# Kernel optimization log

Measured on AMD Instinct MI355X. Metric: run time of the kernel, lower is better.

The kernel has to match this reference:

```python
import jax, jax.numpy as jnp
import numpy as np

T, B, D, R, H = 16, 1024, 1024, 8, 16
DH = D // H


def setup_inputs() -> dict:
    key = jax.random.key(0)
    ks = jax.random.split(key, 10)
    s = 1.0 / np.sqrt(D)
    return {
        "table_embs": jax.random.normal(ks[0], (T, B, D), jnp.float32),
        "rel_embs": jax.random.normal(ks[1], (T, R, D), jnp.float32),
        "rel_idx": jax.random.randint(ks[2], (T, R), 0, T),
        "Wq": jax.random.normal(ks[3], (D, D), jnp.float32) * s,
        "bq": jnp.zeros((D,), jnp.float32),
        "Wk": jax.random.normal(ks[4], (D, D), jnp.float32) * s,
        "bk": jnp.zeros((D,), jnp.float32),
        "Wv": jax.random.normal(ks[5], (D, D), jnp.float32) * s,
        "bv": jnp.zeros((D,), jnp.float32),
        "Wo": jax.random.normal(ks[6], (D, D), jnp.float32) * s,
        "bo": jnp.zeros((D,), jnp.float32),
        "w_rel": jax.random.normal(ks[7], (D,), jnp.float32) * s,
        "b_rel": jnp.zeros((1,), jnp.float32),
    }


def reference(table_embs, rel_embs, rel_idx, Wq, bq, Wk, bk, Wv, bv, Wo, bo, w_rel, b_rel):
    # relationship weights: sigmoid(Linear(rel_emb)) -> scalar per (table, relation)
    rel_w = jax.nn.sigmoid(rel_embs @ w_rel + b_rel[0])          # [T, R]
    # gather related tables' embeddings and apply relationship weight
    others = table_embs[rel_idx]                                  # [T, R, B, D]
    weighted = others * rel_w[:, :, None, None]                   # [T, R, B, D]
    kv_src = jnp.transpose(weighted, (0, 2, 1, 3))                # [T, B, R, D]
    # MultiheadAttention, q_len=1, kv_len=R (PyTorch convention: x @ W.T + b)
    q = (table_embs @ Wq.T + bq).reshape(T, B, H, DH)             # [T, B, H, DH]
    k = (kv_src @ Wk.T + bk).reshape(T, B, R, H, DH)              # [T, B, R, H, DH]
    v = (kv_src @ Wv.T + bv).reshape(T, B, R, H, DH)
    scores = jnp.einsum("tbhd,tbrhd->tbhr", q, k) / np.sqrt(DH)   # [T, B, H, R]
    attn = jax.nn.softmax(scores, axis=-1)
    ctx = jnp.einsum("tbhr,tbrhd->tbhd", attn, v).reshape(T, B, D)
    return ctx @ Wo.T + bo                                        # [T, B, D]
```

## Files before the change

kernel.cpp:

```cpp
#include <hip/hip_runtime.h>


typedef unsigned short u16;
typedef __attribute__((ext_vector_type(8))) short short8;
typedef __attribute__((ext_vector_type(4))) float f32x4;

__device__ __forceinline__ float bf2f(u16 u) {
  unsigned int x = ((unsigned int)u) << 16;
  return __uint_as_float(x);
}
__device__ __forceinline__ u16 f2bf(float f) {
  unsigned int x = __float_as_uint(f);
  unsigned int r = (x + 0x7fffu + ((x >> 16) & 1u)) >> 16;
  return (u16)r;
}

__device__ __forceinline__ void gld_lds16(const void* g, void* l) {
  __builtin_amdgcn_global_load_lds(
      (const __attribute__((address_space(1))) unsigned int*)(unsigned long long)g,
      (__attribute__((address_space(3))) unsigned int*)(unsigned int)(unsigned long long)l,
      16, 0, 0);
}

#define VWAIT(N) asm volatile("s_waitcnt vmcnt(" #N ")" ::: "memory")


__global__ void relw_kernel(const float* __restrict__ rel_embs,
                            const float* __restrict__ w_rel,
                            const float* __restrict__ b_rel,
                            float* __restrict__ rel_w) {
  const int tr = blockIdx.x;
  const float* row = rel_embs + (size_t)tr * 1024;
  const int lane = threadIdx.x;
  float s = 0.f;
  for (int i = lane; i < 1024; i += 64) s += row[i] * w_rel[i];
  for (int off = 32; off > 0; off >>= 1) s += __shfl_down(s, off, 64);
  if (lane == 0) rel_w[tr] = 1.f / (1.f + __expf(-(s + b_rel[0])));
}

__global__ void cvt_f32_bf16(const float* __restrict__ in, u16* __restrict__ out, int n4) {
  int i = blockIdx.x * blockDim.x + threadIdx.x;
  if (i >= n4) return;
  float4 v = ((const float4*)in)[i];
  ushort4 o;
  o.x = f2bf(v.x); o.y = f2bf(v.y); o.z = f2bf(v.z); o.w = f2bf(v.w);
  ((ushort4*)out)[i] = o;
}

__global__ void cvt_w4(const float* __restrict__ Wq, const float* __restrict__ Wk,
                       const float* __restrict__ Wv, const float* __restrict__ Wo,
                       u16* __restrict__ Wcat, u16* __restrict__ Wob) {
  const int i = blockIdx.x * 256 + threadIdx.x;
  const int w = i >> 18;
  const int j = i & 0x3ffff;
  const float* src = (w == 0) ? Wq : (w == 1) ? Wk : (w == 2) ? Wv : Wo;
  u16* dst = (w == 3) ? Wob : (Wcat + ((size_t)w << 20));
  float4 v = ((const float4*)src)[j];
  ushort4 o;
  o.x = f2bf(v.x); o.y = f2bf(v.y); o.z = f2bf(v.z); o.w = f2bf(v.w);
  ((ushort4*)dst)[j] = o;
}


__device__ __forceinline__ void mainloop256(const u16* __restrict__ A,
                                            const u16* __restrict__ B,
                                            u16* lds, int m0, int n0,
                                            f32x4 (&acc)[8][4]) {
  const int tid  = threadIdx.x;
  const int lane = tid & 63;
  const int w    = tid >> 6;
  const int wm   = w >> 2, wn = w & 3;
  const int fr   = lane & 15, fq = lane >> 4;
  const int swz  = fr & 7;

  const unsigned A0 = 0, B0 = 16384, A1 = 32768, B1 = 49152;

  const int srow = tid >> 3;
  const int lc   = (tid & 7) ^ (srow & 7);
  const u16* a0p = A + (size_t)(m0 + srow) * 1024 + lc * 8;
  const u16* b0p = B + (size_t)(n0 + srow) * 1024 + lc * 8;
  const unsigned d0 = (unsigned)((tid & ~63) * 8);

  const u16 *ap0[2], *ap1[2], *bp0[2], *bp1[2];
#pragma unroll
  for (int ks = 0; ks < 2; ++ks) {
    const unsigned ck = (unsigned)((((ks << 2) + fq) ^ swz) << 3);
    ap0[ks] = lds + A0 + (wm * 128 + fr) * 64 + ck;
    ap1[ks] = lds + A1 + (wm * 128 + fr) * 64 + ck;
    bp0[ks] = lds + B0 + (wn * 64 + fr) * 64 + ck;
    bp1[ks] = lds + B1 + (wn * 64 + fr) * 64 + ck;
  }

  short8 afA[4], afB[4], bfr[2][8];

#define STAGE_B4(BO)                                                           \
  do {                                                                         \
    gld_lds16(b0p + 0 * 65536, lds + (BO) + d0 + 0 * 4096);                    \
    gld_lds16(b0p + 1 * 65536, lds + (BO) + d0 + 1 * 4096);                    \
    gld_lds16(b0p + 2 * 65536, lds + (BO) + d0 + 2 * 4096);                    \
    gld_lds16(b0p + 3 * 65536, lds + (BO) + d0 + 3 * 4096);                    \
    b0p += 64;                                                                 \
  } while (0)

#define STAGE_A2(ra, rb, AO)                                                   \
  do {                                                                         \
    gld_lds16(a0p + (ra) * 65536, lds + (AO) + d0 + (ra) * 4096);              \
    gld_lds16(a0p + (rb) * 65536, lds + (AO) + d0 + (rb) * 4096);              \
  } while (0)

#define RD_A(dst, ap, q)                                                       \
  do {                                                                         \
    dst[0] = *(const short8*)((ap)[0] + (2*(q))   * 1024);                     \
    dst[1] = *(const short8*)((ap)[0] + (2*(q)+1) * 1024);                     \
    dst[2] = *(const short8*)((ap)[1] + (2*(q))   * 1024);                     \
    dst[3] = *(const short8*)((ap)[1] + (2*(q)+1) * 1024);                     \
  } while (0)

#define RD_B(TB, bp)                                                           \
  _Pragma("unroll")                                                            \
  for (int j = 0; j < 4; ++j) {                                                \
    bfr[TB][2*j]   = *(const short8*)((bp)[0] + j * 1024);                     \
    bfr[TB][2*j+1] = *(const short8*)((bp)[1] + j * 1024);                     \
  }

#define MFMA_PH(q, S, TB)                                                      \
  do {                                                                         \
    __builtin_amdgcn_s_setprio(1);                                             \
    _Pragma("unroll")                                                          \
    for (int j = 0; j < 4; ++j) {                                              \
      acc[2*(q)][j]   = __builtin_amdgcn_mfma_f32_16x16x32_bf16(S[0], bfr[TB][2*j], acc[2*(q)][j],   0, 0, 0); \
      acc[2*(q)+1][j] = __builtin_amdgcn_mfma_f32_16x16x32_bf16(S[1], bfr[TB][2*j], acc[2*(q)+1][j], 0, 0, 0); \
    }                                                                          \
    _Pragma("unroll")                                                          \
    for (int j = 0; j < 4; ++j) {                                              \
      acc[2*(q)][j]   = __builtin_amdgcn_mfma_f32_16x16x32_bf16(S[2], bfr[TB][2*j+1], acc[2*(q)][j],   0, 0, 0); \
      acc[2*(q)+1][j] = __builtin_amdgcn_mfma_f32_16x16x32_bf16(S[3], bfr[TB][2*j+1], acc[2*(q)+1][j], 0, 0, 0); \
    }                                                                          \
    __builtin_amdgcn_s_setprio(0);                                             \
  } while (0)

#define KTILE(apC, apN, bpN, TBC, TBN, AO_N, BO_N)                             \
  do {                                                                         \
                               \
    RD_A(afB, apC, 1);                                                         \
    STAGE_B4(BO_N);                                                            \
    MFMA_PH(0, afA, TBC);                                                      \
    VWAIT(4);                                         \
    __builtin_amdgcn_s_barrier();                                              \
                                          \
    RD_A(afA, apC, 2);                                                         \
    STAGE_A2(0, 2, AO_N);                                                      \
    MFMA_PH(1, afB, TBC);                                                      \
    __builtin_amdgcn_s_barrier();                                              \
                                          \
    RD_A(afB, apC, 3);                                                         \
    STAGE_A2(1, 3, AO_N); a0p += 64;                                           \
    MFMA_PH(2, afA, TBC);                                                      \
    VWAIT(2);                                      \
    __builtin_amdgcn_s_barrier();                                              \
                         \
    RD_A(afA, apN, 0);                                                         \
    RD_B(TBN, bpN);                                                            \
    MFMA_PH(3, afB, TBC);                                                      \
    __builtin_amdgcn_s_barrier();                                              \
  } while (0)

#define KTILE_LAST(apC, TBC)                                                   \
  do {                                                                         \
    RD_A(afB, apC, 1);                                                         \
    MFMA_PH(0, afA, TBC);                                                      \
    VWAIT(0);                                                                  \
    __builtin_amdgcn_s_barrier();                                              \
    RD_A(afA, apC, 2);                                                         \
    MFMA_PH(1, afB, TBC);                                                      \
    __builtin_amdgcn_s_barrier();                                              \
    RD_A(afB, apC, 3);                                                         \
    MFMA_PH(2, afA, TBC);                                                      \
    __builtin_amdgcn_s_barrier();                                              \
    MFMA_PH(3, afB, TBC);                                                      \
  } while (0)

  gld_lds16(b0p + 0 * 65536, lds + B0 + d0 + 0 * 4096);
  gld_lds16(b0p + 1 * 65536, lds + B0 + d0 + 1 * 4096);
  gld_lds16(b0p + 2 * 65536, lds + B0 + d0 + 2 * 4096);
  gld_lds16(b0p + 3 * 65536, lds + B0 + d0 + 3 * 4096);
  gld_lds16(a0p + 0 * 65536, lds + A0 + d0 + 0 * 4096);
  gld_lds16(a0p + 2 * 65536, lds + A0 + d0 + 2 * 4096);
  gld_lds16(a0p + 1 * 65536, lds + A0 + d0 + 1 * 4096);
  gld_lds16(a0p + 3 * 65536, lds + A0 + d0 + 3 * 4096);
  a0p += 64; b0p += 64;
  VWAIT(2);
  __builtin_amdgcn_s_barrier();
  RD_B(0, bp0);
  RD_A(afA, ap0, 0);

  for (int it = 0; it < 7; ++it) {
    KTILE(ap0, ap1, bp1, 0, 1, A1, B1);
    KTILE(ap1, ap0, bp0, 1, 0, A0, B0);
  }
  KTILE(ap0, ap1, bp1, 0, 1, A1, B1);
  KTILE_LAST(ap1, 1);

#undef STAGE_B4
#undef STAGE_A2
#undef RD_A
#undef RD_B
#undef MFMA_PH
#undef KTILE
#undef KTILE_LAST
}

__device__ __forceinline__ void xcd_swizzle(int nx, int ny, int& bx, int& by) {
  const int nwg = nx * ny;
  int bid = by * nx + bx;
  bid = (bid & 7) * (nwg >> 3) + (bid >> 3);
  bx = bid % nx;
  by = bid / nx;
}

__global__ __launch_bounds__(512, 1)
void gemm_qkv(const u16* __restrict__ A, const u16* __restrict__ Bw,
              const float* __restrict__ bq,
              u16* __restrict__ Qt, u16* __restrict__ Kt, u16* __restrict__ Vt) {
  __shared__ __align__(16) u16 lds[65536];
  int bx = blockIdx.x, by = blockIdx.y;
  xcd_swizzle(gridDim.x, gridDim.y, bx, by);
  const int n0 = bx * 256;
  const int m0 = by * 256;
  f32x4 acc[8][4];
#pragma unroll
  for (int i = 0; i < 8; ++i)
#pragma unroll
    for (int j = 0; j < 4; ++j) acc[i][j] = (f32x4){0.f, 0.f, 0.f, 0.f};

  mainloop256(A, Bw, lds, m0, n0, acc);
  __syncthreads();

  const int tid  = threadIdx.x;
  const int lane = tid & 63;
  const int w    = tid >> 6;
  const int wm   = w >> 2, wn = w & 3;
  const int colw = lane & 15, roww = (lane >> 4) * 4;
  const int t = m0 >> 10, b0 = m0 & 1023;
  const int sel = n0 >> 10, dbase = n0 & 1023;
  u16* outp = (sel == 0) ? Qt : (sel == 1) ? Kt : Vt;

  {
    char* reg = (char*)(lds + wm * 32768);
#pragma unroll
    for (int j = 0; j < 4; ++j) {
      const int dl = wn * 64 + j * 16 + colw;
      const float badd = (sel == 0) ? bq[dbase + dl] : 0.f;
      char* rowp = reg + (unsigned)dl * 256;
      const unsigned sx = ((unsigned)dl & 7) << 4;
#pragma unroll
      for (int i = 0; i < 8; ++i) {
        const int bl = i * 16 + roww;
        uint2 pv;
        pv.x = (unsigned)f2bf(acc[i][j][0] + badd)
             | ((unsigned)f2bf(acc[i][j][1] + badd) << 16);
        pv.y = (unsigned)f2bf(acc[i][j][2] + badd)
             | ((unsigned)f2bf(acc[i][j][3] + badd) << 16);
        *(uint2*)(rowp + (((unsigned)bl * 2) ^ sx)) = pv;
      }
    }
  }
  __syncthreads();
#pragma unroll
  for (int pass = 0; pass < 2; ++pass) {
    const char* regp = (const char*)(lds + pass * 32768);
#pragma unroll
    for (int rr = 0; rr < 8; ++rr) {
      const int slot = rr * 512 + tid;
      const int row = slot >> 4, c16 = slot & 15;
      const uint4 v = *(const uint4*)(regp + (unsigned)row * 256
                                      + (((unsigned)c16 * 16) ^ (((unsigned)row & 7) << 4)));
      *(uint4*)(outp + ((size_t)t << 20) + (size_t)(dbase + row) * 1024
                + b0 + pass * 128 + c16 * 8) = v;
    }
  }
}

__global__ __launch_bounds__(512, 1)
void gemm_out(const u16* __restrict__ A, const u16* __restrict__ Bw,
              const float* __restrict__ bo, float* __restrict__ out) {
  __shared__ __align__(16) u16 lds[65536];
  int bx = blockIdx.x, by = blockIdx.y;
  xcd_swizzle(gridDim.x, gridDim.y, bx, by);
  const int n0 = bx * 256;
  const int m0 = by * 256;
  f32x4 acc[8][4];
#pragma unroll
  for (int i = 0; i < 8; ++i)
#pragma unroll
    for (int j = 0; j < 4; ++j) acc[i][j] = (f32x4){0.f, 0.f, 0.f, 0.f};

  mainloop256(A, Bw, lds, m0, n0, acc);

  const int lane = threadIdx.x & 63;
  const int w    = threadIdx.x >> 6;
  const int wm   = w >> 2, wn = w & 3;
  const int colw = lane & 15, roww = (lane >> 4) * 4;
#pragma unroll
  for (int j = 0; j < 4; ++j) {
    const int gn = n0 + wn * 64 + j * 16 + colw;
    const float bov = bo[gn];
#pragma unroll
    for (int i = 0; i < 8; ++i) {
      const int gm = m0 + wm * 128 + i * 16 + roww;
#pragma unroll
      for (int r = 0; r < 4; ++r)
        out[(size_t)(gm + r) * 1024 + gn] = acc[i][j][r] + bov;
    }
  }
}

__global__ __launch_bounds__(256)
void attn5(const u16* __restrict__ Qt, const u16* __restrict__ Kt,
           const u16* __restrict__ Vt,
           const float* __restrict__ relw, const int* __restrict__ rel_idx,
           const float* __restrict__ bk, const float* __restrict__ bv,
           u16* __restrict__ ctx) {
  const int tid = threadIdx.x;
  const int h = blockIdx.y, t = blockIdx.z;
  const int b0 = blockIdx.x * 256;
  const int b = b0 + tid;
  const int hd = h * 64;

  __shared__ u16  st[256 * 34];
  __shared__ float bks[64], bvs[64], rws[8];
  __shared__ int   rids[8];

  if (tid < 64) { bks[tid] = bk[hd + tid]; bvs[tid] = bv[hd + tid]; }
  else if (tid < 72) { rws[tid - 64] = relw[t * 8 + (tid - 64)];
                       rids[tid - 64] = rel_idx[t * 8 + (tid - 64)]; }
  __syncthreads();

  const unsigned qoff = ((unsigned)t << 20) + ((unsigned)hd << 10) + (unsigned)b;
  unsigned koff[8];
#pragma unroll
  for (int r = 0; r < 8; ++r)
    koff[r] = ((unsigned)rids[r] << 20) + ((unsigned)hd << 10) + (unsigned)b;

  float acc[8];
#pragma unroll
  for (int r = 0; r < 8; ++r) acc[r] = 0.f;
  float qbk = 0.f;
#pragma unroll 4
  for (int d = 0; d < 64; ++d) {
    const float q = bf2f(Qt[qoff + d * 1024]);
    qbk += q * bks[d];
#pragma unroll
    for (int r = 0; r < 8; ++r)
      acc[r] += q * bf2f(Kt[koff[r] + d * 1024]);
  }

  float w[8];
  {
    float s[8], mx = -1e30f;
#pragma unroll
    for (int r = 0; r < 8; ++r) {
      s[r] = (rws[r] * acc[r] + qbk) * 0.125f;
      mx = fmaxf(mx, s[r]);
    }
    float sum = 0.f;
#pragma unroll
    for (int r = 0; r < 8; ++r) { s[r] = __expf(s[r] - mx); sum += s[r]; }
    const float inv = 1.f / sum;
#pragma unroll
    for (int r = 0; r < 8; ++r) w[r] = s[r] * inv * rws[r];
  }

  for (int half = 0; half < 2; ++half) {
#pragma unroll
    for (int dp = 0; dp < 32; dp += 2) {
      const int d = half * 32 + dp;
      float o0 = bvs[d];
      float o1 = bvs[d + 1];
#pragma unroll
      for (int r = 0; r < 8; ++r) {
        o0 += w[r] * bf2f(Vt[koff[r] + d * 1024]);
        o1 += w[r] * bf2f(Vt[koff[r] + (d + 1) * 1024]);
      }
      const unsigned p = (unsigned)f2bf(o0) | ((unsigned)f2bf(o1) << 16);
      *(unsigned*)(st + tid * 34 + dp) = p;
    }
    __syncthreads();
    {
      const int sub = tid & 7;
      const int rbase = tid >> 3;
#pragma unroll
      for (int p = 0; p < 8; ++p) {
        const int row = p * 32 + rbase;
        const uint2 v = *(const uint2*)(st + row * 34 + sub * 4);
        *(uint2*)(ctx + ((size_t)(t * 1024 + b0 + row)) * 1024
                  + hd + half * 32 + sub * 4) = v;
      }
    }
    __syncthreads();
  }
}


extern "C" void kernel_launch(void* const* d_in, const int* in_sizes, int n_in,
                              void* d_out, int out_size, void* d_ws, size_t ws_size,
                              hipStream_t stream) {
  const float* table = (const float*)d_in[0];
  const float* rele  = (const float*)d_in[1];
  const int*   ridx  = (const int*)d_in[2];
  const float* Wq    = (const float*)d_in[3];
  const float* bq    = (const float*)d_in[4];
  const float* Wk    = (const float*)d_in[5];
  const float* bk    = (const float*)d_in[6];
  const float* Wv    = (const float*)d_in[7];
  const float* bv    = (const float*)d_in[8];
  const float* Wo    = (const float*)d_in[9];
  const float* bo    = (const float*)d_in[10];
  const float* wr    = (const float*)d_in[11];
  const float* br    = (const float*)d_in[12];
  float* out = (float*)d_out;

  char* ws = (char*)d_ws;
  const size_t MB = 1024 * 1024;
  u16*  Xbf  = (u16*)(ws);
  u16*  Kt   = (u16*)(ws + 32  * MB);
  u16*  Vt   = (u16*)(ws + 64  * MB);
  u16*  Qt   = (u16*)(ws + 96  * MB);
  u16*  Wcat = (u16*)(ws + 128 * MB);
  u16*  Wob  = (u16*)(ws + 134 * MB);
  float* relw = (float*)(ws + 136 * MB);
  u16*  ctxb = Xbf;

  relw_kernel<<<128, 64, 0, stream>>>(rele, wr, br, relw);
  cvt_f32_bf16<<<16384, 256, 0, stream>>>(table, Xbf, 4194304);
  cvt_w4<<<4096, 256, 0, stream>>>(Wq, Wk, Wv, Wo, Wcat, Wob);

  gemm_qkv<<<dim3(12, 64), 512, 0, stream>>>(Xbf, Wcat, bq, Qt, Kt, Vt);
  attn5<<<dim3(4, 16, 16), 256, 0, stream>>>(Qt, Kt, Vt, relw, ridx, bk, bv, ctxb);
  gemm_out<<<dim3(4, 64), 512, 0, stream>>>(ctxb, Wob, bo, out);
}
```

Measured before the change: 368.8 us.

## Hand-schedule LDS fragment reads with inline ds_read and explicit lgkmcnt waits

Replaces compiler-generated LDS loads in the GEMM main loop with inline-asm ds_read_b128 that use immediate offsets from precomputed byte bases. Explicit lgkmcnt waits and sched_barriers pin the order of the reads and the MFMA phases. Next-tile B fragment reads are split across phases 2 and 3, and a vmcnt wait is added in phase 1. The aim is to cut address arithmetic and conservative compiler waitcnts so LDS reads overlap with MFMAs. The compiler cannot track the asm loads, so correctness now depends entirely on the hand-placed waits.

Result: no change. 371.7 us (+0.8%).

```diff
diff --git a/kernel.cpp b/kernel.cpp
--- a/kernel.cpp
+++ b/kernel.cpp
@@ -22,7 +22,14 @@
       16, 0, 0);
 }
 
-#define VWAIT(N) asm volatile("s_waitcnt vmcnt(" #N ")" ::: "memory")
+#define STR_(x) #x
+#define STR(x) STR_(x)
+#define VWAIT(N) asm volatile("s_waitcnt vmcnt(" STR(N) ")" ::: "memory")
+#define LWAIT(N) asm volatile("s_waitcnt lgkmcnt(" STR(N) ")" ::: "memory")
+#define SCHED0   __builtin_amdgcn_sched_barrier(0)
+#define DSR(dst, base, OFF)                                                    \
+  asm volatile("ds_read_b128 %0, %1 offset:" STR(OFF)                          \
+               : "=v"(dst) : "v"(base))
 
 
 __global__ void relw_kernel(const float* __restrict__ rel_embs,
@@ -81,14 +88,16 @@
   const u16* b0p = B + (size_t)(n0 + srow) * 1024 + lc * 8;
   const unsigned d0 = (unsigned)((tid & ~63) * 8);
 
-  const u16 *ap0[2], *ap1[2], *bp0[2], *bp1[2];
-#pragma unroll
-  for (int ks = 0; ks < 2; ++ks) {
-    const unsigned ck = (unsigned)((((ks << 2) + fq) ^ swz) << 3);
-    ap0[ks] = lds + A0 + (wm * 128 + fr) * 64 + ck;
-    ap1[ks] = lds + A1 + (wm * 128 + fr) * 64 + ck;
-    bp0[ks] = lds + B0 + (wn * 64 + fr) * 64 + ck;
-    bp1[ks] = lds + B1 + (wn * 64 + fr) * 64 + ck;
+  unsigned uA0k0, uA0k1, uA1k0, uA1k1, uB0k0, uB0k1, uB1k0, uB1k1;
+  {
+    const unsigned ck0 = (unsigned)(((0 + fq) ^ swz) << 3);
+    const unsigned ck1 = (unsigned)(((4 + fq) ^ swz) << 3);
+    const unsigned ar = (unsigned)((wm * 128 + fr) * 64);
+    const unsigned br = (unsigned)((wn * 64 + fr) * 64);
+    uA0k0 = (A0 + ar + ck0) * 2;  uA0k1 = (A0 + ar + ck1) * 2;
+    uA1k0 = (A1 + ar + ck0) * 2;  uA1k1 = (A1 + ar + ck1) * 2;
+    uB0k0 = (B0 + br + ck0) * 2;  uB0k1 = (B0 + br + ck1) * 2;
+    uB1k0 = (B1 + br + ck0) * 2;  uB1k1 = (B1 + br + ck1) * 2;
   }
 
   short8 afA[4], afB[4], bfr[2][8];
@@ -108,20 +117,17 @@
     gld_lds16(a0p + (rb) * 65536, lds + (AO) + d0 + (rb) * 4096);              \
   } while (0)
 
-#define RD_A(dst, ap, q)                                                       \
-  do {                                                                         \
-    dst[0] = *(const short8*)((ap)[0] + (2*(q))   * 1024);                     \
-    dst[1] = *(const short8*)((ap)[0] + (2*(q)+1) * 1024);                     \
-    dst[2] = *(const short8*)((ap)[1] + (2*(q))   * 1024);                     \
-    dst[3] = *(const short8*)((ap)[1] + (2*(q)+1) * 1024);                     \
-  } while (0)
-
-#define RD_B(TB, bp)                                                           \
-  _Pragma("unroll")                                                            \
-  for (int j = 0; j < 4; ++j) {                                                \
-    bfr[TB][2*j]   = *(const short8*)((bp)[0] + j * 1024);                     \
-    bfr[TB][2*j+1] = *(const short8*)((bp)[1] + j * 1024);                     \
-  }
+#define RD_A2(dst, bk0, bk1, O0, O1)                                           \
+  do {                                                                         \
+    DSR(dst[0], bk0, O0); DSR(dst[1], bk0, O1);                                \
+    DSR(dst[2], bk1, O0); DSR(dst[3], bk1, O1);                                \
+  } while (0)
+
+#define RD_B2(TB, bk0, bk1, O0, O1, I0)                                        \
+  do {                                                                         \
+    DSR(bfr[TB][(I0)+0], bk0, O0); DSR(bfr[TB][(I0)+1], bk1, O0);              \
+    DSR(bfr[TB][(I0)+2], bk0, O1); DSR(bfr[TB][(I0)+3], bk1, O1);              \
+  } while (0)
 
 #define MFMA_PH(q, S, TB)                                                      \
   do {                                                                         \
@@ -139,44 +145,56 @@
     __builtin_amdgcn_s_setprio(0);                                             \
   } while (0)
 
-#define KTILE(apC, apN, bpN, TBC, TBN, AO_N, BO_N)                             \
-  do {                                                                         \
-                               \
-    RD_A(afB, apC, 1);                                                         \
+#define BAR __builtin_amdgcn_s_barrier()
+
+#define KTILE(aC0, aC1, aN0, aN1, bN0, bN1, TBC, TBN, AO_N, BO_N)              \
+  do {                                                                         \
+                         \
+    RD_A2(afB, aC0, aC1, 4096, 6144);                                          \
     STAGE_B4(BO_N);                                                            \
-    MFMA_PH(0, afA, TBC);                                                      \
+    LWAIT(4); SCHED0;                                                          \
+    MFMA_PH(0, afA, TBC); SCHED0;                                              \
     VWAIT(4);                                         \
-    __builtin_amdgcn_s_barrier();                                              \
-                                          \
-    RD_A(afA, apC, 2);                                                         \
+    BAR;                                                                       \
+                        \
+    RD_A2(afA, aC0, aC1, 8192, 10240);                                         \
     STAGE_A2(0, 2, AO_N);                                                      \
-    MFMA_PH(1, afB, TBC);                                                      \
-    __builtin_amdgcn_s_barrier();                                              \
-                                          \
-    RD_A(afB, apC, 3);                                                         \
+    LWAIT(4); SCHED0;                                                          \
+    MFMA_PH(1, afB, TBC); SCHED0;                                              \
+    VWAIT(2);                                               \
+    BAR;                                                                       \
+         \
+    RD_A2(afB, aC0, aC1, 12288, 14336);                                        \
+    RD_B2(TBN, bN0, bN1, 0, 2048, 0);                                          \
     STAGE_A2(1, 3, AO_N); a0p += 64;                                           \
-    MFMA_PH(2, afA, TBC);                                                      \
-    VWAIT(2);                                      \
-    __builtin_amdgcn_s_barrier();                                              \
-                         \
-    RD_A(afA, apN, 0);                                                         \
-    RD_B(TBN, bpN);                                                            \
-    MFMA_PH(3, afB, TBC);                                                      \
-    __builtin_amdgcn_s_barrier();                                              \
-  } while (0)
-
-#define KTILE_LAST(apC, TBC)                                                   \
-  do {                                                                         \
-    RD_A(afB, apC, 1);                                                         \
-    MFMA_PH(0, afA, TBC);                                                      \
+    LWAIT(8); SCHED0;                                                          \
+    MFMA_PH(2, afA, TBC); SCHED0;                                              \
+    VWAIT(2);                                         \
+    BAR;                                                                       \
+                   \
+    RD_A2(afA, aN0, aN1, 0, 2048);                                             \
+    RD_B2(TBN, bN0, bN1, 4096, 6144, 4);                                       \
+    LWAIT(8); SCHED0;                                                          \
+    MFMA_PH(3, afB, TBC); SCHED0;                                              \
+    BAR;                                                                       \
+  } while (0)
+
+#define KTILE_LAST(aC0, aC1, TBC)                                              \
+  do {                                                                         \
+    RD_A2(afB, aC0, aC1, 4096, 6144);                                          \
+    LWAIT(4); SCHED0;                                                          \
+    MFMA_PH(0, afA, TBC); SCHED0;                                              \
     VWAIT(0);                                                                  \
-    __builtin_amdgcn_s_barrier();                                              \
-    RD_A(afA, apC, 2);                                                         \
-    MFMA_PH(1, afB, TBC);                                                      \
-    __builtin_amdgcn_s_barrier();                                              \
-    RD_A(afB, apC, 3);                                                         \
-    MFMA_PH(2, afA, TBC);                                                      \
-    __builtin_amdgcn_s_barrier();                                              \
+    BAR;                                                                       \
+    RD_A2(afA, aC0, aC1, 8192, 10240);                                         \
+    LWAIT(4); SCHED0;                                                          \
+    MFMA_PH(1, afB, TBC); SCHED0;                                              \
+    BAR;                                                                       \
+    RD_A2(afB, aC0, aC1, 12288, 14336);                                        \
+    LWAIT(4); SCHED0;                                                          \
+    MFMA_PH(2, afA, TBC); SCHED0;                                              \
+    BAR;                                                                       \
+    LWAIT(0); SCHED0;                                                          \
     MFMA_PH(3, afB, TBC);                                                      \
   } while (0)
 
@@ -190,22 +208,24 @@
   gld_lds16(a0p + 3 * 65536, lds + A0 + d0 + 3 * 4096);
   a0p += 64; b0p += 64;
   VWAIT(2);
-  __builtin_amdgcn_s_barrier();
-  RD_B(0, bp0);
-  RD_A(afA, ap0, 0);
+  BAR;
+  RD_B2(0, uB0k0, uB0k1, 0, 2048, 0);
+  RD_B2(0, uB0k0, uB0k1, 4096, 6144, 4);
+  RD_A2(afA, uA0k0, uA0k1, 0, 2048);
 
   for (int it = 0; it < 7; ++it) {
-    KTILE(ap0, ap1, bp1, 0, 1, A1, B1);
-    KTILE(ap1, ap0, bp0, 1, 0, A0, B0);
-  }
-  KTILE(ap0, ap1, bp1, 0, 1, A1, B1);
-  KTILE_LAST(ap1, 1);
+    KTILE(uA0k0, uA0k1, uA1k0, uA1k1, uB1k0, uB1k1, 0, 1, A1, B1);
+    KTILE(uA1k0, uA1k1, uA0k0, uA0k1, uB0k0, uB0k1, 1, 0, A0, B0);
+  }
+  KTILE(uA0k0, uA0k1, uA1k0, uA1k1, uB1k0, uB1k1, 0, 1, A1, B1);
+  KTILE_LAST(uA1k0, uA1k1, 1);
 
 #undef STAGE_B4
 #undef STAGE_A2
-#undef RD_A
-#undef RD_B
+#undef RD_A2
+#undef RD_B2
 #undef MFMA_PH
+#undef BAR
 #undef KTILE
 #undef KTILE_LAST
 }
```
